# Performance work log

Measured on AMD Instinct MI355X. Metric: run time of the kernel, lower is better.

The kernel has to match this reference:

```python
import jax, jax.numpy as jnp
import numpy as np

B, R, N, K, E = 128, 500, 500, 10, 128
H1 = 5 * E  # UnvisitedMLP hidden = embedding_dim * 5


def setup_inputs() -> dict:
    key = jax.random.key(0)
    ks = jax.random.split(key, 8)
    current = jax.random.randint(ks[0], (B, R), 0, N)
    distance = jax.random.uniform(ks[1], (B, N, N), dtype=jnp.float32)
    # unvisited cities, exercising the padding-index path in search_unvisited.
    visited = jax.random.uniform(ks[2], (B, R, N)) < 0.97
    masked = jnp.where(visited, -jnp.inf, 0.0).astype(jnp.float32)
    encoded_nodes = jax.random.normal(ks[3], (B, N, E), dtype=jnp.float32)
    w1 = jax.random.normal(ks[4], (H1, K * E), dtype=jnp.float32) * (1.0 / np.sqrt(K * E))
    b1 = jnp.zeros((H1,), dtype=jnp.float32)
    w2 = jax.random.normal(ks[5], (E, H1), dtype=jnp.float32) * (1.0 / np.sqrt(H1))
    b2 = jnp.zeros((E,), dtype=jnp.float32)
    return {"current": current, "distance": distance, "masked": masked,
            "encoded_nodes": encoded_nodes, "w1": w1, "b1": b1, "w2": w2, "b2": b2}


def _search_unvisited(current, distance, masked, k_near):
    # distance_filtered[b, r, :] = distance[b, current[b, r], :]  -> [B, R, N]
    b_idx = jnp.arange(current.shape[0])[:, None]
    distance_filtered = distance[b_idx, current, :]
    mask_unvisited = masked != -jnp.inf
    distance_masked = jnp.where(mask_unvisited, distance_filtered, jnp.inf)
    # k smallest == top-k of negated distances
    neg_vals, k_idx = jax.lax.top_k(-distance_masked, k_near)  # [B, R, K]
    is_inf = neg_vals == -jnp.inf  # entries that were +inf (no unvisited left)
    n_cities = distance.shape[1]
    return jnp.where(is_inf, n_cities, k_idx)  # padding index = problem_size


def _gather_pad0(encoded_nodes, idx):
    # pad encoded_nodes with a zero row at index N, then gather  -> [B, R, K, E]
    padded = jnp.concatenate(
        [encoded_nodes, jnp.zeros_like(encoded_nodes[:, :1, :])], axis=1)
    b_idx = jnp.arange(encoded_nodes.shape[0])[:, None, None]
    return padded[b_idx, idx, :]


def _pad_avg(a):
    # replace all-zero (padding) rows along K with the mean of non-zero rows
    is_zero = a.sum(axis=-1) == 0  # [B, R, K]
    nz_count = jnp.clip((~is_zero).sum(axis=-1).astype(jnp.float32), 1e-9)
    mean_vec = a.sum(axis=2) / nz_count[..., None]  # [B, R, E]
    return jnp.where(is_zero[..., None], mean_vec[:, :, None, :], a)


def reference(current, distance, masked, encoded_nodes, w1, b1, w2, b2):
    k_near = K
    idx = _search_unvisited(current, distance, masked, k_near)  # [B, R, K]
    emb = _gather_pad0(encoded_nodes, idx)                      # [B, R, K, E]
    emb = _pad_avg(emb)
    h = emb.reshape(emb.shape[0], emb.shape[1], k_near * emb.shape[-1])  # [B, R, K*E]
    h = jax.nn.relu(jnp.einsum('brf,hf->brh', h, w1) + b1)
    out = jnp.einsum('brh,eh->bre', h, w2) + b2  # [B, R, E]
    return out
```

## Files before the change

### kernel.cpp

```cpp
#include <hip/hip_runtime.h>
#include <cstdint>
#include <cstddef>

#define Bn   128
#define Rn   500
#define Nn   500
#define Kn   10
#define En   128
#define H1n  640
#define KEn  1280
#define Mn   (Bn * Rn)

typedef short s16x8 __attribute__((ext_vector_type(8)));
typedef float f32x4 __attribute__((ext_vector_type(4)));

__device__ __forceinline__ unsigned short f2bf(float x) {
    union { float f; unsigned int u; } v; v.f = x;
    unsigned int r = v.u + 0x7fffu + ((v.u >> 16) & 1u);
    return (unsigned short)(r >> 16);
}
__device__ __forceinline__ float bf2f(unsigned short u) {
    union { unsigned int u; float f; } v; v.u = ((unsigned int)u) << 16;
    return v.f;
}
__device__ __forceinline__ void gl2lds16(const void* g, void* l) {
    __builtin_amdgcn_global_load_lds(
        (const __attribute__((address_space(1))) unsigned int*)g,
        (__attribute__((address_space(3))) unsigned int*)l, 16, 0, 0);
}
__device__ __forceinline__ void drain_all() {
    asm volatile("s_waitcnt vmcnt(0) lgkmcnt(0)" ::: "memory");
}
#define WAITV(n) asm volatile("s_waitcnt vmcnt(" #n ")" ::: "memory")
__device__ __forceinline__ void pipe_barrier() {
    __builtin_amdgcn_s_barrier();
    asm volatile("" ::: "memory");
}

__global__ void convw_kernel(const float* __restrict__ enc, const float* __restrict__ w1,
                             const float* __restrict__ w2,
                             unsigned short* __restrict__ encb, unsigned short* __restrict__ w1b,
                             unsigned short* __restrict__ w2b) {
    int i = blockIdx.x * 256 + threadIdx.x;
    if (i < (Bn * Nn * En) / 4) {
        float4 v = ((const float4*)enc)[i];
        ushort4 o; o.x = f2bf(v.x); o.y = f2bf(v.y); o.z = f2bf(v.z); o.w = f2bf(v.w);
        ((ushort4*)encb)[i] = o;
    }
    if (i < (H1n * KEn) / 4) {
        float4 v = ((const float4*)w1)[i];
        ushort4 o; o.x = f2bf(v.x); o.y = f2bf(v.y); o.z = f2bf(v.z); o.w = f2bf(v.w);
        ((ushort4*)w1b)[i] = o;
    }
    if (i < (En * H1n) / 4) {
        float4 v = ((const float4*)w2)[i];
        ushort4 o; o.x = f2bf(v.x); o.y = f2bf(v.y); o.z = f2bf(v.z); o.w = f2bf(v.w);
        ((ushort4*)w2b)[i] = o;
    }
}

__global__ __launch_bounds__(256) void select_kernel(const int* __restrict__ current,
                            const float* __restrict__ distance,
                            const float* __restrict__ masked,
                            const unsigned short* __restrict__ encb,
                            int* __restrict__ idx_out,
                            unsigned short* __restrict__ meanbb) {
    const int row  = blockIdx.x * 4 + (threadIdx.x >> 6);
    const int lane = threadIdx.x & 63;
    const int b    = row / Rn;
    const int cur  = current[row];
    const unsigned int* drow = (const unsigned int*)(distance + ((size_t)b * Nn + cur) * Nn);
    const unsigned int* mrow = (const unsigned int*)(masked + (size_t)row * Nn);

    unsigned long long key[8];
#pragma unroll
    for (int i = 0; i < 8; ++i) {
        int nn = lane + 64 * i;
        unsigned int fb = 0x7F800000u;
        if (nn < Nn) {
            unsigned int m = mrow[nn];
            unsigned int d = drow[nn];
            fb = (m == 0xFF800000u) ? 0x7F800000u : d;
        }
        key[i] = ((unsigned long long)fb << 32) | (unsigned int)nn;
    }

    int ids[Kn];
    int myid = Nn;
#pragma unroll
    for (int it = 0; it < Kn; ++it) {
        unsigned long long bk = key[0];
#pragma unroll
        for (int i = 1; i < 8; ++i) bk = (key[i] < bk) ? key[i] : bk;
#pragma unroll
        for (int off = 1; off < 64; off <<= 1) {
            unsigned long long ok = __shfl_xor(bk, off);
            bk = (ok < bk) ? ok : bk;
        }
        const int wid = ((bk >> 32) == 0x7F800000u) ? Nn : (int)(bk & 0xffffffffu);
        ids[it] = wid;
        if (lane == it) myid = wid;
#pragma unroll
        for (int i = 0; i < 8; ++i)
            if (key[i] == bk) key[i] = 0x7F800000FFFFFFFFull;
    }
    if (lane < Kn) idx_out[row * Kn + lane] = myid;

    const unsigned int* encu = (const unsigned int*)(encb + (size_t)b * Nn * En);
    float s0 = 0.f, s1 = 0.f; int cnt = 0;
#pragma unroll
    for (int k = 0; k < Kn; ++k) {
        const int id = ids[k];
        if (id < Nn) {
            unsigned int u = encu[id * (En / 2) + lane];
            s0 += bf2f((unsigned short)(u & 0xffffu));
            s1 += bf2f((unsigned short)(u >> 16));
            cnt++;
        }
    }
    float m0 = 0.f, m1 = 0.f;
    if (cnt > 0) { m0 = s0 / (float)cnt; m1 = s1 / (float)cnt; }
    unsigned int packed = (unsigned int)f2bf(m0) | ((unsigned int)f2bf(m1) << 16);
    ((unsigned int*)meanbb)[(size_t)row * (En / 2) + lane] = packed;
}

__global__ __launch_bounds__(512, 4) void gemm1_kernel(
        const unsigned short* __restrict__ encb, const unsigned short* __restrict__ meanbb,
        const int* __restrict__ idxb, const unsigned short* __restrict__ w1b,
        const float* __restrict__ b1, unsigned short* __restrict__ hbuf) {
    extern __shared__ unsigned short lds[];
    unsigned short* const As   = lds;
    unsigned short* const Bs   = lds + 3 * 256 * 32;
    unsigned short* const idxs = lds + 3 * 256 * 32 + 3 * 128 * 32;

    const int p  = blockIdx.x;
    const int x  = p & 7;
    const int rk = p >> 3;
    const int w  = (x < 2 ? x * 157 : 314 + (x - 2) * 156) + rk;
    const int row0 = (w / 5) * 256;
    const int h0   = (w % 5) * 128;

    const int t    = threadIdx.x;
    const int lane = t & 63;
    const int wave = t >> 6;
    const int ln15 = lane & 15;
    const int q4   = lane >> 4;
    const int wm4  = wave & 3;
    const int wn   = wave >> 2;

    for (int i = t; i < 256 * Kn; i += 512)
        idxs[i] = (unsigned short)idxb[row0 * Kn + i];

    const int rl   = lane >> 2;
    const int sc   = lane & 3;
    const int coff = (sc ^ (rl & 3)) * 8;

    int lrowA[2];
    const unsigned short* encB[2];
    const unsigned short* meanR[2];
#pragma unroll
    for (int s = 0; s < 2; ++s) {
        lrowA[s] = wave * 32 + s * 16 + rl;
        const int gr = row0 + lrowA[s];
        encB[s]  = encb + (size_t)(gr / Rn) * Nn * En;
        meanR[s] = meanbb + (size_t)gr * En + coff;
    }
    const int lrowB = wave * 16 + rl;
    const unsigned short* w1R = w1b + (size_t)(h0 + lrowB) * KEn + coff;

    f32x4 acc[4][4];
#pragma unroll
    for (int i = 0; i < 4; ++i)
#pragma unroll
        for (int j = 0; j < 4; ++j)
            acc[i][j] = (f32x4){0.f, 0.f, 0.f, 0.f};

    auto issueA = [&](int kt, int cb) {
        const int j  = kt >> 2;
        const int e0 = (kt & 3) * 32;
#pragma unroll
        for (int s = 0; s < 2; ++s) {
            const int id = idxs[lrowA[s] * Kn + j];
            const unsigned short* src = (id < Nn)
                ? (encB[s] + (size_t)id * En + e0 + coff)
                : (meanR[s] + e0);
            gl2lds16(src, As + (size_t)cb * (256 * 32) + (wave * 32 + s * 16) * 32);
        }
    };
    auto issueB = [&](int kt, int cb) {
        gl2lds16(w1R + kt * 32, Bs + (size_t)cb * (128 * 32) + (wave * 16) * 32);
    };

    drain_all();
    __syncthreads();
    issueA(0, 0); issueB(0, 0);
    issueA(1, 1); issueB(1, 1);
    WAITV(3);
    pipe_barrier();

    const int rA  = wm4 * 64 + ln15;
    const int rB  = wn  * 64 + ln15;
    const int slA = (q4 ^ (rA & 3)) * 8;
    const int slB = (q4 ^ (rB & 3)) * 8;

#define MFMA16(a, bvec, c) c = __builtin_amdgcn_mfma_f32_16x16x32_bf16(a, bvec, c, 0, 0, 0)

#pragma unroll
    for (int kt = 0; kt < 40; ++kt) {
        const int cb = kt % 3;
        const unsigned short* Ab = As + cb * (256 * 32);
        const unsigned short* Bb = Bs + cb * (128 * 32);
        s16x8 af0, af1, af2, af3, bq0, bq1;

        af0 = *(const s16x8*)(Ab + (rA +  0) * 32 + slA);
        af1 = *(const s16x8*)(Ab + (rA + 16) * 32 + slA);
        af2 = *(const s16x8*)(Ab + (rA + 32) * 32 + slA);
        af3 = *(const s16x8*)(Ab + (rA + 48) * 32 + slA);
        bq0 = *(const s16x8*)(Bb + (rB +  0) * 32 + slB);
        bq1 = *(const s16x8*)(Bb + (rB + 16) * 32 + slB);
        if (kt + 2 < 40) issueA(kt + 2, (kt + 2) % 3);
        pipe_barrier();
        __builtin_amdgcn_s_setprio(1);
        MFMA16(af0, bq0, acc[0][0]); MFMA16(af1, bq0, acc[1][0]);
        MFMA16(af2, bq0, acc[2][0]); MFMA16(af3, bq0, acc[3][0]);
        MFMA16(af0, bq1, acc[0][1]); MFMA16(af1, bq1, acc[1][1]);
        MFMA16(af2, bq1, acc[2][1]); MFMA16(af3, bq1, acc[3][1]);
        __builtin_amdgcn_s_setprio(0);
        pipe_barrier();

        bq0 = *(const s16x8*)(Bb + (rB + 32) * 32 + slB);
        bq1 = *(const s16x8*)(Bb + (rB + 48) * 32 + slB);
        if (kt + 2 < 40) issueB(kt + 2, (kt + 2) % 3);
        pipe_barrier();
        __builtin_amdgcn_s_setprio(1);
        MFMA16(af0, bq0, acc[0][2]); MFMA16(af1, bq0, acc[1][2]);
        MFMA16(af2, bq0, acc[2][2]); MFMA16(af3, bq0, acc[3][2]);
        MFMA16(af0, bq1, acc[0][3]); MFMA16(af1, bq1, acc[1][3]);
        MFMA16(af2, bq1, acc[2][3]); MFMA16(af3, bq1, acc[3][3]);
        __builtin_amdgcn_s_setprio(0);
        if (kt + 2 < 40)      { WAITV(3); }
        else if (kt + 1 < 40) { WAITV(0); }
        pipe_barrier();
    }
#undef MFMA16

#pragma unroll
    for (int i = 0; i < 4; ++i) {
#pragma unroll
        for (int jj = 0; jj < 4; ++jj) {
            const int h = h0 + wn * 64 + jj * 16 + ln15;
            const float bias = b1[h];
#pragma unroll
            for (int rg = 0; rg < 4; ++rg) {
                const int m = wm4 * 64 + i * 16 + q4 * 4 + rg;
                float vv = acc[i][jj][rg] + bias;
                vv = fmaxf(vv, 0.f);
                hbuf[(size_t)(row0 + m) * H1n + h] = f2bf(vv);
            }
        }
    }
}

__global__ __launch_bounds__(256, 4) void gemm2_kernel(
        const unsigned short* __restrict__ hbuf, const unsigned short* __restrict__ w2b,
        const float* __restrict__ b2, float* __restrict__ out) {
    __shared__ alignas(16) unsigned short As[3][128 * 32];
    __shared__ alignas(16) unsigned short Bs[3][128 * 32];

    const int row0 = blockIdx.x * 128;
    const int t    = threadIdx.x;
    const int lane = t & 63;
    const int wave = t >> 6;
    const int ln15 = lane & 15;
    const int q4   = lane >> 4;
    const int wm   = wave & 1;
    const int wn   = wave >> 1;

    const int rl   = lane >> 2;
    const int sc   = lane & 3;
    const int coff = (sc ^ (rl & 3)) * 8;

    const unsigned short* hrow[2];
    const unsigned short* w2row[2];
#pragma unroll
    for (int s = 0; s < 2; ++s) {
        const int lr = wave * 32 + s * 16 + rl;
        hrow[s]  = hbuf + (size_t)(row0 + lr) * H1n + coff;
        w2row[s] = w2b + (size_t)lr * H1n + coff;
    }

    f32x4 acc[4][4];
#pragma unroll
    for (int i = 0; i < 4; ++i)
#pragma unroll
        for (int j = 0; j < 4; ++j)
            acc[i][j] = (f32x4){0.f, 0.f, 0.f, 0.f};

    auto issueA = [&](int kt, int cb) {
#pragma unroll
        for (int s = 0; s < 2; ++s)
            gl2lds16(hrow[s] + kt * 32, &As[cb][(wave * 32 + s * 16) * 32]);
    };
    auto issueB = [&](int kt, int cb) {
#pragma unroll
        for (int s = 0; s < 2; ++s)
            gl2lds16(w2row[s] + kt * 32, &Bs[cb][(wave * 32 + s * 16) * 32]);
    };

    issueA(0, 0); issueB(0, 0);
    issueA(1, 1); issueB(1, 1);
    WAITV(4);
    pipe_barrier();

    const int rA  = wm * 64 + ln15;
    const int rB  = wn * 64 + ln15;
    const int slA = (q4 ^ (rA & 3)) * 8;
    const int slB = (q4 ^ (rB & 3)) * 8;

#define MFMA16(a, bvec, c) c = __builtin_amdgcn_mfma_f32_16x16x32_bf16(a, bvec, c, 0, 0, 0)

#pragma unroll
    for (int kt = 0; kt < 20; ++kt) {
        const int cb = kt % 3;
        const unsigned short* Ab = As[cb];
        const unsigned short* Bb = Bs[cb];
        s16x8 af0, af1, af2, af3, bq0, bq1;

        af0 = *(const s16x8*)(Ab + (rA +  0) * 32 + slA);
        af1 = *(const s16x8*)(Ab + (rA + 16) * 32 + slA);
        af2 = *(const s16x8*)(Ab + (rA + 32) * 32 + slA);
        af3 = *(const s16x8*)(Ab + (rA + 48) * 32 + slA);
        bq0 = *(const s16x8*)(Bb + (rB +  0) * 32 + slB);
        bq1 = *(const s16x8*)(Bb + (rB + 16) * 32 + slB);
        if (kt + 2 < 20) issueA(kt + 2, (kt + 2) % 3);
        pipe_barrier();
        __builtin_amdgcn_s_setprio(1);
        MFMA16(af0, bq0, acc[0][0]); MFMA16(af1, bq0, acc[1][0]);
        MFMA16(af2, bq0, acc[2][0]); MFMA16(af3, bq0, acc[3][0]);
        MFMA16(af0, bq1, acc[0][1]); MFMA16(af1, bq1, acc[1][1]);
        MFMA16(af2, bq1, acc[2][1]); MFMA16(af3, bq1, acc[3][1]);
        __builtin_amdgcn_s_setprio(0);
        pipe_barrier();

        bq0 = *(const s16x8*)(Bb + (rB + 32) * 32 + slB);
        bq1 = *(const s16x8*)(Bb + (rB + 48) * 32 + slB);
        if (kt + 2 < 20) issueB(kt + 2, (kt + 2) % 3);
        pipe_barrier();
        __builtin_amdgcn_s_setprio(1);
        MFMA16(af0, bq0, acc[0][2]); MFMA16(af1, bq0, acc[1][2]);
        MFMA16(af2, bq0, acc[2][2]); MFMA16(af3, bq0, acc[3][2]);
        MFMA16(af0, bq1, acc[0][3]); MFMA16(af1, bq1, acc[1][3]);
        MFMA16(af2, bq1, acc[2][3]); MFMA16(af3, bq1, acc[3][3]);
        __builtin_amdgcn_s_setprio(0);
        if (kt + 2 < 20)      { WAITV(4); }
        else if (kt + 1 < 20) { WAITV(0); }
        pipe_barrier();
    }
#undef MFMA16

#pragma unroll
    for (int i = 0; i < 4; ++i) {
#pragma unroll
        for (int jj = 0; jj < 4; ++jj) {
            const int e = wn * 64 + jj * 16 + ln15;
            const float bias = b2[e];
#pragma unroll
            for (int rg = 0; rg < 4; ++rg) {
                const int m = wm * 64 + i * 16 + q4 * 4 + rg;
                out[(size_t)(row0 + m) * En + e] = acc[i][jj][rg] + bias;
            }
        }
    }
}

extern "C" void kernel_launch(void* const* d_in, const int* in_sizes, int n_in,
                              void* d_out, int out_size, void* d_ws, size_t ws_size,
                              hipStream_t stream) {
    const int*   current  = (const int*)d_in[0];
    const float* distance = (const float*)d_in[1];
    const float* masked   = (const float*)d_in[2];
    const float* encoded  = (const float*)d_in[3];
    const float* w1       = (const float*)d_in[4];
    const float* b1       = (const float*)d_in[5];
    const float* w2       = (const float*)d_in[6];
    const float* b2       = (const float*)d_in[7];
    float* out = (float*)d_out;

    char* ws = (char*)d_ws;
    const size_t OFF_IDX  = 0;
    const size_t OFF_ENCB = 2560000;
    const size_t OFF_MEAN = OFF_ENCB + 16384000;
    const size_t OFF_W1B  = OFF_MEAN + 16384000;
    const size_t OFF_W2B  = OFF_W1B + 1638400;
    const size_t OFF_H    = OFF_W2B + 163840;
    int*            idxb   = (int*)(ws + OFF_IDX);
    unsigned short* encb   = (unsigned short*)(ws + OFF_ENCB);
    unsigned short* meanbb = (unsigned short*)(ws + OFF_MEAN);
    unsigned short* w1b    = (unsigned short*)(ws + OFF_W1B);
    unsigned short* w2b    = (unsigned short*)(ws + OFF_W2B);
    unsigned short* hbuf   = (unsigned short*)(ws + OFF_H);

    static bool s_attr = false;
    if (!s_attr) {
        hipFuncSetAttribute(reinterpret_cast<const void*>(gemm1_kernel),
                            hipFuncAttributeMaxDynamicSharedMemorySize, 78848);
        s_attr = true;
    }

    convw_kernel<<<(Bn * Nn * En / 4 + 255) / 256, 256, 0, stream>>>(encoded, w1, w2, encb, w1b, w2b);
    select_kernel<<<Mn / 4, 256, 0, stream>>>(current, distance, masked, encb, idxb, meanbb);
    gemm1_kernel<<<1250, 512, 78848, stream>>>(encb, meanbb, idxb, w1b, b1, hbuf);
    gemm2_kernel<<<Mn / 128, 256, 0, stream>>>(hbuf, w2b, b2, out);
}
```

Before: 467.5 us.

## Compact unvisited candidates and bitonic-sort small sets; change LDS swizzle

The top-k selection first compacts unvisited cities into per-wave shared memory using ballot and prefix counts. When 64 or fewer remain, which is typical at about 3% unvisited, a single 64-lane bitonic sort replaces ten rounds of 8-way min plus shuffle reductions; otherwise it falls back to the old iterative min. It also reads the distance row only for unvisited entries. Separately, the LDS XOR swizzle in both GEMM kernels now uses bits 1-2 of the row instead of bits 0-1, to reduce bank conflicts for 16-byte fragment reads, at the cost of 16KB shared memory in the select kernel.

```diff
diff --git a/kernel.cpp b/kernel.cpp
--- a/kernel.cpp
+++ b/kernel.cpp
@@ -65,46 +65,85 @@
                             const unsigned short* __restrict__ encb,
                             int* __restrict__ idx_out,
                             unsigned short* __restrict__ meanbb) {
-    const int row  = blockIdx.x * 4 + (threadIdx.x >> 6);
+    __shared__ unsigned long long buf[4][512];
+    const int wv   = threadIdx.x >> 6;
+    const int row  = blockIdx.x * 4 + wv;
     const int lane = threadIdx.x & 63;
     const int b    = row / Rn;
     const int cur  = current[row];
     const unsigned int* drow = (const unsigned int*)(distance + ((size_t)b * Nn + cur) * Nn);
     const unsigned int* mrow = (const unsigned int*)(masked + (size_t)row * Nn);
-
-    unsigned long long key[8];
+    unsigned long long* wbuf = buf[wv];
+    const unsigned long long INFKEY = 0x7F800000FFFFFFFFull;
+
+    int n = 0;
 #pragma unroll
     for (int i = 0; i < 8; ++i) {
-        int nn = lane + 64 * i;
-        unsigned int fb = 0x7F800000u;
+        const int nn = lane + 64 * i;
+        bool fin = false;
+        unsigned long long key = 0;
         if (nn < Nn) {
-            unsigned int m = mrow[nn];
-            unsigned int d = drow[nn];
-            fb = (m == 0xFF800000u) ? 0x7F800000u : d;
-        }
-        key[i] = ((unsigned long long)fb << 32) | (unsigned int)nn;
-    }
+            const unsigned int m = mrow[nn];
+            if (m != 0xFF800000u) {
+                const unsigned int d = drow[nn];
+                key = ((unsigned long long)d << 32) | (unsigned int)nn;
+                fin = true;
+            }
+        }
+        const unsigned long long bal = __ballot(fin);
+        const int pfx = (int)__popcll(bal & ((1ull << lane) - 1ull));
+        if (fin) wbuf[n + pfx] = key;
+        n += (int)__popcll(bal);
+    }
+    __syncthreads();
 
     int ids[Kn];
-    int myid = Nn;
-#pragma unroll
-    for (int it = 0; it < Kn; ++it) {
-        unsigned long long bk = key[0];
-#pragma unroll
-        for (int i = 1; i < 8; ++i) bk = (key[i] < bk) ? key[i] : bk;
-#pragma unroll
-        for (int off = 1; off < 64; off <<= 1) {
-            unsigned long long ok = __shfl_xor(bk, off);
-            bk = (ok < bk) ? ok : bk;
-        }
-        const int wid = ((bk >> 32) == 0x7F800000u) ? Nn : (int)(bk & 0xffffffffu);
-        ids[it] = wid;
-        if (lane == it) myid = wid;
-#pragma unroll
-        for (int i = 0; i < 8; ++i)
-            if (key[i] == bk) key[i] = 0x7F800000FFFFFFFFull;
-    }
-    if (lane < Kn) idx_out[row * Kn + lane] = myid;
+    if (n <= 64) {
+        unsigned long long key = (lane < n) ? wbuf[lane] : INFKEY;
+#pragma unroll
+        for (int k = 2; k <= 64; k <<= 1) {
+#pragma unroll
+            for (int j = k >> 1; j >= 1; j >>= 1) {
+                const unsigned long long ok = __shfl_xor(key, j);
+                const bool takemin = (((lane & k) == 0) == ((lane & j) == 0));
+                const unsigned long long mn = (ok < key) ? ok : key;
+                const unsigned long long mx = (ok < key) ? key : ok;
+                key = takemin ? mn : mx;
+            }
+        }
+        const int wid = ((unsigned int)(key >> 32) >= 0x7F800000u) ? Nn
+                                                                   : (int)(key & 0xffffffffu);
+        if (lane < Kn) idx_out[row * Kn + lane] = wid;
+#pragma unroll
+        for (int k = 0; k < Kn; ++k) ids[k] = __shfl(wid, k);
+    } else {
+        unsigned long long key8[8];
+#pragma unroll
+        for (int i = 0; i < 8; ++i) {
+            const int ii = lane + 64 * i;
+            key8[i] = (ii < n) ? wbuf[ii] : INFKEY;
+        }
+        int myid = Nn;
+#pragma unroll
+        for (int it = 0; it < Kn; ++it) {
+            unsigned long long bk = key8[0];
+#pragma unroll
+            for (int i = 1; i < 8; ++i) bk = (key8[i] < bk) ? key8[i] : bk;
+#pragma unroll
+            for (int off = 1; off < 64; off <<= 1) {
+                const unsigned long long ok = __shfl_xor(bk, off);
+                bk = (ok < bk) ? ok : bk;
+            }
+            const int wid = ((unsigned int)(bk >> 32) >= 0x7F800000u) ? Nn
+                                                                      : (int)(bk & 0xffffffffu);
+            ids[it] = wid;
+            if (lane == it) myid = wid;
+#pragma unroll
+            for (int i = 0; i < 8; ++i)
+                if (key8[i] == bk) key8[i] = INFKEY;
+        }
+        if (lane < Kn) idx_out[row * Kn + lane] = myid;
+    }
 
     const unsigned int* encu = (const unsigned int*)(encb + (size_t)b * Nn * En);
     float s0 = 0.f, s1 = 0.f; int cnt = 0;
@@ -153,7 +192,7 @@
 
     const int rl   = lane >> 2;
     const int sc   = lane & 3;
-    const int coff = (sc ^ (rl & 3)) * 8;
+    const int coff = (sc ^ ((rl >> 1) & 3)) * 8;
 
     int lrowA[2];
     const unsigned short* encB[2];
@@ -200,8 +239,8 @@
 
     const int rA  = wm4 * 64 + ln15;
     const int rB  = wn  * 64 + ln15;
-    const int slA = (q4 ^ (rA & 3)) * 8;
-    const int slB = (q4 ^ (rB & 3)) * 8;
+    const int slA = (q4 ^ ((rA >> 1) & 3)) * 8;
+    const int slB = (q4 ^ ((rB >> 1) & 3)) * 8;
 
 #define MFMA16(a, bvec, c) c = __builtin_amdgcn_mfma_f32_16x16x32_bf16(a, bvec, c, 0, 0, 0)
 
@@ -278,7 +317,7 @@
 
     const int rl   = lane >> 2;
     const int sc   = lane & 3;
-    const int coff = (sc ^ (rl & 3)) * 8;
+    const int coff = (sc ^ ((rl >> 1) & 3)) * 8;
 
     const unsigned short* hrow[2];
     const unsigned short* w2row[2];
@@ -314,8 +353,8 @@
 
     const int rA  = wm * 64 + ln15;
     const int rB  = wn * 64 + ln15;
-    const int slA = (q4 ^ (rA & 3)) * 8;
-    const int slB = (q4 ^ (rB & 3)) * 8;
+    const int slA = (q4 ^ ((rA >> 1) & 3)) * 8;
+    const int slB = (q4 ^ ((rB >> 1) & 3)) * 8;
 
 #define MFMA16(a, bvec, c) c = __builtin_amdgcn_mfma_f32_16x16x32_bf16(a, bvec, c, 0, 0, 0)
 
```

New measurement: 499.8 us. 6.9% more time.
